# Optimization experiments

Measured on AMD Instinct MI355X. Metric: run time of the kernel, lower is better.

## Reference

```python
import jax, jax.numpy as jnp
import numpy as np

B, D, C = 256, 512, 100000
U_M, L_M = 0.8, 0.45
U_A, L_A = 110.0, 10.0
LAMBDA_G = 35.0
SCALE = 64.0


def setup_inputs() -> dict:
    key = jax.random.key(0)
    k1, k2, k3, k4 = jax.random.split(key, 4)
    x = jax.random.normal(k1, (B, D), dtype=jnp.float32)
    # per-sample feature magnitudes in [l_a, u_a]
    x_norm = L_A + jax.random.uniform(k2, (B, 1), dtype=jnp.float32) * (U_A - L_A)
    labels = jax.random.randint(k3, (B,), 0, C)
    weight = jax.random.normal(k4, (C, D), dtype=jnp.float32)
    return {"x": x, "x_norm": x_norm, "labels": labels, "weight": weight}


def reference(x, x_norm, labels, weight):
    # adaptive margin m(a) = slope * (a - l_a) + l_m, per sample [B,1]
    ada_margin = (U_M - L_M) / (U_A - L_A) * (x_norm - L_A) + L_M
    cos_m = jnp.cos(ada_margin)
    sin_m = jnp.sin(ada_margin)

    xn = x / jnp.linalg.norm(x, axis=-1, keepdims=True)          # [B,D]
    wn = weight / jnp.linalg.norm(weight, axis=-1, keepdims=True)  # [C,D]
    cos_theta = jnp.clip(jnp.einsum('bd,cd->bc', xn, wn), -1.0, 1.0)  # [B,C]
    sin_theta = jnp.sqrt(1.0 - cos_theta * cos_theta)
    cos_theta_m = cos_theta * cos_m - sin_theta * sin_m
    # easy_margin=True: only apply margin where cos_theta > 0
    cos_theta_m = jnp.where(cos_theta > 0, cos_theta_m, cos_theta)

    one_hot = jax.nn.one_hot(labels, C, dtype=cos_theta.dtype)   # [B,C]
    logits = SCALE * (one_hot * cos_theta_m + (1.0 - one_hot) * cos_theta)

    # cross-entropy with mean reduction
    tgt = jnp.take_along_axis(logits, labels[:, None], axis=1)[:, 0]
    ce = jnp.mean(jax.nn.logsumexp(logits, axis=1) - tgt)

    # MagFace G-loss: mean(a / u_a^2 + 1/a)
    loss_g = jnp.mean(x_norm / (U_A * U_A) + 1.0 / x_norm)
    return ce + LAMBDA_G * loss_g
```

## Files before the change

kernel.cpp:

```cpp
#include <hip/hip_runtime.h>
#include <hip/hip_bf16.h>

#define BB 256
#define DD 512
#define CNUM 100000
#define CPAD 100096
#define NCHUNK 782
#define NPART (NCHUNK * 2)

typedef __attribute__((ext_vector_type(8))) short bf16x8;
typedef __attribute__((ext_vector_type(4))) float f32x4;

typedef __attribute__((address_space(1))) void gvoid_t;
typedef __attribute__((address_space(3))) void lvoid_t;

__device__ __forceinline__ void gload16(const void* g, void* l) {
  __builtin_amdgcn_global_load_lds((const gvoid_t*)g, (lvoid_t*)l, 16, 0, 0);
}

__device__ __forceinline__ unsigned short f2bf(float f) {
  union { float f; unsigned int u; } v; v.f = f;
  unsigned int u = v.u;
  unsigned int r = u + 0x7FFFu + ((u >> 16) & 1u);
  return (unsigned short)(r >> 16);
}

__global__ void k_prep_x(const float* __restrict__ x, const float* __restrict__ xnrm,
                         unsigned short* __restrict__ xn, float* __restrict__ cm,
                         float* __restrict__ sm) {
  int b = blockIdx.x;
  int lane = threadIdx.x;
  const float4* xr = (const float4*)(x + (size_t)b * DD);
  float4 v0 = xr[lane * 2];
  float4 v1 = xr[lane * 2 + 1];
  float ss = v0.x * v0.x + v0.y * v0.y + v0.z * v0.z + v0.w * v0.w +
             v1.x * v1.x + v1.y * v1.y + v1.z * v1.z + v1.w * v1.w;
#pragma unroll
  for (int msk = 1; msk < 64; msk <<= 1) ss += __shfl_xor(ss, msk, 64);
  float inv = rsqrtf(ss);
  unsigned int p0 = (unsigned int)f2bf(v0.x * inv) | ((unsigned int)f2bf(v0.y * inv) << 16);
  unsigned int p1 = (unsigned int)f2bf(v0.z * inv) | ((unsigned int)f2bf(v0.w * inv) << 16);
  unsigned int p2 = (unsigned int)f2bf(v1.x * inv) | ((unsigned int)f2bf(v1.y * inv) << 16);
  unsigned int p3 = (unsigned int)f2bf(v1.z * inv) | ((unsigned int)f2bf(v1.w * inv) << 16);
  *(uint4*)(xn + (size_t)b * DD + lane * 8) = make_uint4(p0, p1, p2, p3);
  if (lane == 0) {
    float a = xnrm[b];
    float marg = 0.0035f * (a - 10.0f) + 0.45f;
    cm[b] = cosf(marg);
    sm[b] = sinf(marg);
  }
}

__global__ __launch_bounds__(512) void k_gemm(
    const unsigned short* __restrict__ xn, const float* __restrict__ w,
    const int* __restrict__ labels, const float* __restrict__ cmv,
    const float* __restrict__ smv, float2* __restrict__ part, float* __restrict__ tgt) {
  __shared__ short Xs[BB * 64];
  __shared__ short Ws[128 * 64];
  __shared__ float sInvW[128];
  __shared__ int sLab[BB];
  __shared__ float sCm[BB], sSm[BB];

  int tid = threadIdx.x, wave = tid >> 6, lane = tid & 63;
  int wm = wave >> 1, wq = wave & 1;
  int cbase = blockIdx.x * 128;

  if (tid < BB) {
    sLab[tid] = labels[tid];
    sCm[tid] = cmv[tid];
    sSm[tid] = smv[tid];
  }
  __syncthreads();

  int lr = lane >> 3;
  int lk = (lane & 7) ^ lr;

  int wrow = tid >> 2, wseg = tid & 3;
  int wr_clamped = cbase + wrow;
  if (wr_clamped >= CNUM) wr_clamped = 0;
  const float* wptr = w + (size_t)wr_clamped * DD + wseg * 16;
  float ssacc = 0.0f;
  int wsw0 = wrow * 64 + ((wseg * 16) ^ ((wrow & 7) << 3));
  int wsw1 = wrow * 64 + ((wseg * 16 + 8) ^ ((wrow & 7) << 3));

  f32x4 acc[4][4];
#pragma unroll
  for (int m = 0; m < 4; ++m)
#pragma unroll
    for (int n = 0; n < 4; ++n) acc[m][n] = (f32x4){0.f, 0.f, 0.f, 0.f};

  f32x4 wv[4];
#pragma unroll
  for (int j = 0; j < 4; ++j) wv[j] = *(const f32x4*)(wptr + j * 4);

#pragma unroll
  for (int kc = 0; kc < 8; ++kc) {
    const int k0 = kc * 64;
    asm volatile("s_barrier" ::: "memory");
#pragma unroll
    for (int i = 0; i < 4; ++i) {
      int rbase = i * 64 + wave * 8;
      gload16(xn + (size_t)(rbase + lr) * DD + k0 + lk * 8, &Xs[rbase * 64]);
    }
    asm volatile("s_waitcnt vmcnt(4)" ::: "memory");
    {
      f32x4 a = wv[0], b = wv[1], c = wv[2], d = wv[3];
      ssacc += a[0]*a[0] + a[1]*a[1] + a[2]*a[2] + a[3]*a[3] +
               b[0]*b[0] + b[1]*b[1] + b[2]*b[2] + b[3]*b[3] +
               c[0]*c[0] + c[1]*c[1] + c[2]*c[2] + c[3]*c[3] +
               d[0]*d[0] + d[1]*d[1] + d[2]*d[2] + d[3]*d[3];
      unsigned int q0 = (unsigned int)f2bf(a[0]) | ((unsigned int)f2bf(a[1]) << 16);
      unsigned int q1 = (unsigned int)f2bf(a[2]) | ((unsigned int)f2bf(a[3]) << 16);
      unsigned int q2 = (unsigned int)f2bf(b[0]) | ((unsigned int)f2bf(b[1]) << 16);
      unsigned int q3 = (unsigned int)f2bf(b[2]) | ((unsigned int)f2bf(b[3]) << 16);
      unsigned int q4 = (unsigned int)f2bf(c[0]) | ((unsigned int)f2bf(c[1]) << 16);
      unsigned int q5 = (unsigned int)f2bf(c[2]) | ((unsigned int)f2bf(c[3]) << 16);
      unsigned int q6 = (unsigned int)f2bf(d[0]) | ((unsigned int)f2bf(d[1]) << 16);
      unsigned int q7 = (unsigned int)f2bf(d[2]) | ((unsigned int)f2bf(d[3]) << 16);
      *(uint4*)&Ws[wsw0] = make_uint4(q0, q1, q2, q3);
      *(uint4*)&Ws[wsw1] = make_uint4(q4, q5, q6, q7);
    }
    if (kc < 7) {
#pragma unroll
      for (int j = 0; j < 4; ++j) wv[j] = *(const f32x4*)(wptr + (kc + 1) * 64 + j * 4);
      asm volatile("s_waitcnt vmcnt(4) lgkmcnt(0)" ::: "memory");
    } else {
      asm volatile("s_waitcnt vmcnt(0) lgkmcnt(0)" ::: "memory");
    }
    asm volatile("s_barrier" ::: "memory");
#pragma unroll
    for (int ks = 0; ks < 2; ++ks) {
      int krd = ks * 32 + (lane >> 4) * 8;
      int swz = (lane & 7) << 3;
      bf16x8 af[4], bfr[4];
#pragma unroll
      for (int m = 0; m < 4; ++m) {
        int ra = wm * 64 + m * 16 + (lane & 15);
        af[m] = *(const bf16x8*)&Xs[ra * 64 + (krd ^ swz)];
      }
#pragma unroll
      for (int n = 0; n < 4; ++n) {
        int rb = wq * 64 + n * 16 + (lane & 15);
        bfr[n] = *(const bf16x8*)&Ws[rb * 64 + (krd ^ swz)];
      }
#pragma unroll
      for (int m = 0; m < 4; ++m)
#pragma unroll
        for (int n = 0; n < 4; ++n)
          acc[m][n] = __builtin_amdgcn_mfma_f32_16x16x32_bf16(af[m], bfr[n], acc[m][n], 0, 0, 0);
    }
  }

  ssacc += __shfl_xor(ssacc, 1, 64);
  ssacc += __shfl_xor(ssacc, 2, 64);
  if (wseg == 0) sInvW[wrow] = rsqrtf(ssacc);
  __syncthreads();

  int g = lane >> 4, cb = lane & 15;
  float invc[4];
#pragma unroll
  for (int n = 0; n < 4; ++n) {
    int col = cbase + wq * 64 + n * 16 + cb;
    invc[n] = (col < CNUM) ? sInvW[wq * 64 + n * 16 + cb] : 0.0f;
  }
#pragma unroll
  for (int m = 0; m < 4; ++m) {
#pragma unroll
    for (int r = 0; r < 4; ++r) {
      int row = wm * 64 + m * 16 + g * 4 + r;
      int lab = sLab[row];
      float cmr = sCm[row], smr = sSm[row];
      float lg[4];
      float vmax = -1e30f;
#pragma unroll
      for (int n = 0; n < 4; ++n) {
        int col = cbase + wq * 64 + n * 16 + cb;
        float cv = acc[m][n][r] * invc[n];
        cv = fminf(1.0f, fmaxf(-1.0f, cv));
        float logit;
        if (col == lab) {
          float st = sqrtf(fmaxf(0.0f, 1.0f - cv * cv));
          float cm2 = cv * cmr - st * smr;
          logit = 64.0f * (cv > 0.0f ? cm2 : cv);
          tgt[row] = logit;
        } else {
          logit = 64.0f * cv;
        }
        if (col >= CNUM) logit = -1e30f;
        lg[n] = logit;
        vmax = fmaxf(vmax, logit);
      }
#pragma unroll
      for (int msk = 1; msk < 16; msk <<= 1) vmax = fmaxf(vmax, __shfl_xor(vmax, msk, 64));
      float s = 0.0f;
#pragma unroll
      for (int n = 0; n < 4; ++n) s += __expf(lg[n] - vmax);
#pragma unroll
      for (int msk = 1; msk < 16; msk <<= 1) s += __shfl_xor(s, msk, 64);
      if (cb == 0) part[(size_t)row * NPART + blockIdx.x * 2 + wq] = make_float2(vmax, s);
    }
  }
}

__global__ void k_merge(const float2* __restrict__ part, const float* __restrict__ tgt,
                        float* __restrict__ ce) {
  int b = blockIdx.x, t = threadIdx.x;
  float m = -1e30f, s = 0.0f;
  for (int i = t; i < NPART; i += 256) {
    float2 p = part[(size_t)b * NPART + i];
    float nm = fmaxf(m, p.x);
    s = s * __expf(m - nm) + p.y * __expf(p.x - nm);
    m = nm;
  }
  __shared__ float smx[256], ssm[256];
  smx[t] = m;
  ssm[t] = s;
  __syncthreads();
  for (int off = 128; off > 0; off >>= 1) {
    if (t < off) {
      float m2 = smx[t + off], s2 = ssm[t + off];
      float nm = fmaxf(smx[t], m2);
      ssm[t] = ssm[t] * __expf(smx[t] - nm) + s2 * __expf(m2 - nm);
      smx[t] = nm;
    }
    __syncthreads();
  }
  if (t == 0) ce[b] = smx[0] + logf(ssm[0]) - tgt[b];
}

__global__ void k_final(const float* __restrict__ ce, const float* __restrict__ xnrm,
                        float* __restrict__ out) {
  int t = threadIdx.x;
  float cv = ce[t];
  float a = xnrm[t];
  float gv = a * (1.0f / (110.0f * 110.0f)) + 1.0f / a;
  __shared__ float s1[256], s2[256];
  s1[t] = cv;
  s2[t] = gv;
  __syncthreads();
  for (int off = 128; off > 0; off >>= 1) {
    if (t < off) {
      s1[t] += s1[t + off];
      s2[t] += s2[t + off];
    }
    __syncthreads();
  }
  if (t == 0) out[0] = s1[0] * (1.0f / 256.0f) + 35.0f * s2[0] * (1.0f / 256.0f);
}

extern "C" void kernel_launch(void* const* d_in, const int* in_sizes, int n_in,
                              void* d_out, int out_size, void* d_ws, size_t ws_size,
                              hipStream_t stream) {
  const float* x = (const float*)d_in[0];
  const float* xnrm = (const float*)d_in[1];
  const int* labels = (const int*)d_in[2];
  const float* w = (const float*)d_in[3];

  char* ws = (char*)d_ws;
  unsigned short* XN = (unsigned short*)ws;
  size_t off = (size_t)BB * DD * 2;
  float* CM = (float*)(ws + off);  off += 1024;
  float* SM = (float*)(ws + off);  off += 1024;
  float* TGT = (float*)(ws + off); off += 1024;
  float* CE = (float*)(ws + off);  off += 1024;
  float2* PART = (float2*)(ws + off);

  k_prep_x<<<BB, 64, 0, stream>>>(x, xnrm, XN, CM, SM);
  k_gemm<<<NCHUNK, 512, 0, stream>>>(XN, w, labels, CM, SM, PART, TGT);
  k_merge<<<BB, 256, 0, stream>>>(PART, TGT, CE);
  k_final<<<1, 256, 0, stream>>>(CE, xnrm, (float*)d_out);
}
```

Baseline: 100.5 us.

## Split GEMM over batch halves and double-buffer LDS tiles

The GEMM grid gains a second dimension that splits the 256 batch rows into two 128-row tiles. Each block now computes a 128x128 output tile with 8 waves arranged 2x4, and the number of softmax partials per row doubles. X and W tiles in LDS are double-buffered so the next k-chunk loads while MFMAs run on the current one. The cost is that every W tile is read from global memory and converted to bf16 twice, once per batch half, doubling W traffic, which may dominate because W is large.

Result: no change. 102.1 us (+1.6%).

```diff
diff --git a/kernel.cpp b/kernel.cpp
--- a/kernel.cpp
+++ b/kernel.cpp
@@ -5,8 +5,10 @@
 #define DD 512
 #define CNUM 100000
 #define CPAD 100096
-#define NCHUNK 782
-#define NPART (NCHUNK * 2)
+#define BM 128
+#define BN 128
+#define NCH_N 782
+#define NPART (NCH_N * 4)
 
 typedef __attribute__((ext_vector_type(8))) short bf16x8;
 typedef __attribute__((ext_vector_type(4))) float f32x4;
@@ -55,20 +57,21 @@
     const unsigned short* __restrict__ xn, const float* __restrict__ w,
     const int* __restrict__ labels, const float* __restrict__ cmv,
     const float* __restrict__ smv, float2* __restrict__ part, float* __restrict__ tgt) {
-  __shared__ short Xs[BB * 64];
-  __shared__ short Ws[128 * 64];
-  __shared__ float sInvW[128];
-  __shared__ int sLab[BB];
-  __shared__ float sCm[BB], sSm[BB];
+  __shared__ short Xs[2][BM * 64];
+  __shared__ short Ws[2][BN * 64];
+  __shared__ float sInvW[BN];
+  __shared__ int sLab[BM];
+  __shared__ float sCm[BM], sSm[BM];
 
   int tid = threadIdx.x, wave = tid >> 6, lane = tid & 63;
-  int wm = wave >> 1, wq = wave & 1;
-  int cbase = blockIdx.x * 128;
-
-  if (tid < BB) {
-    sLab[tid] = labels[tid];
-    sCm[tid] = cmv[tid];
-    sSm[tid] = smv[tid];
+  int wm = wave >> 2, wq = wave & 3;
+  int cbase = blockIdx.x * BN;
+  int mbase = blockIdx.y * BM;
+
+  if (tid < BM) {
+    sLab[tid] = labels[mbase + tid];
+    sCm[tid] = cmv[mbase + tid];
+    sSm[tid] = smv[mbase + tid];
   }
   __syncthreads();
 
@@ -76,80 +79,101 @@
   int lk = (lane & 7) ^ lr;
 
   int wrow = tid >> 2, wseg = tid & 3;
-  int wr_clamped = cbase + wrow;
-  if (wr_clamped >= CNUM) wr_clamped = 0;
-  const float* wptr = w + (size_t)wr_clamped * DD + wseg * 16;
+  int wr_c = cbase + wrow;
+  if (wr_c >= CNUM) wr_c = 0;
+  const float* wptr = w + (size_t)wr_c * DD + wseg * 16;
   float ssacc = 0.0f;
   int wsw0 = wrow * 64 + ((wseg * 16) ^ ((wrow & 7) << 3));
   int wsw1 = wrow * 64 + ((wseg * 16 + 8) ^ ((wrow & 7) << 3));
 
-  f32x4 acc[4][4];
+  f32x4 acc[4][2];
 #pragma unroll
   for (int m = 0; m < 4; ++m)
 #pragma unroll
-    for (int n = 0; n < 4; ++n) acc[m][n] = (f32x4){0.f, 0.f, 0.f, 0.f};
+    for (int n = 0; n < 2; ++n) acc[m][n] = (f32x4){0.f, 0.f, 0.f, 0.f};
+
+#define STAGE_X(T, B)                                                          \
+  {                                                                            \
+    const int k0_ = (T) * 64;                                                  \
+    _Pragma("unroll") for (int i = 0; i < 2; ++i) {                            \
+      int rbase = i * 64 + wave * 8;                                           \
+      gload16(xn + (size_t)(mbase + rbase + lr) * DD + k0_ + lk * 8,           \
+              &Xs[B][rbase * 64]);                                             \
+    }                                                                          \
+  }
+
+#define PACK_W(B)                                                              \
+  {                                                                            \
+    f32x4 a = wv[0], b = wv[1], c = wv[2], d = wv[3];                          \
+    ssacc += a[0]*a[0] + a[1]*a[1] + a[2]*a[2] + a[3]*a[3] +                   \
+             b[0]*b[0] + b[1]*b[1] + b[2]*b[2] + b[3]*b[3] +                   \
+             c[0]*c[0] + c[1]*c[1] + c[2]*c[2] + c[3]*c[3] +                   \
+             d[0]*d[0] + d[1]*d[1] + d[2]*d[2] + d[3]*d[3];                    \
+    unsigned int q0 = (unsigned int)f2bf(a[0]) | ((unsigned int)f2bf(a[1]) << 16); \
+    unsigned int q1 = (unsigned int)f2bf(a[2]) | ((unsigned int)f2bf(a[3]) << 16); \
+    unsigned int q2 = (unsigned int)f2bf(b[0]) | ((unsigned int)f2bf(b[1]) << 16); \
+    unsigned int q3 = (unsigned int)f2bf(b[2]) | ((unsigned int)f2bf(b[3]) << 16); \
+    unsigned int q4 = (unsigned int)f2bf(c[0]) | ((unsigned int)f2bf(c[1]) << 16); \
+    unsigned int q5 = (unsigned int)f2bf(c[2]) | ((unsigned int)f2bf(c[3]) << 16); \
+    unsigned int q6 = (unsigned int)f2bf(d[0]) | ((unsigned int)f2bf(d[1]) << 16); \
+    unsigned int q7 = (unsigned int)f2bf(d[2]) | ((unsigned int)f2bf(d[3]) << 16); \
+    *(uint4*)&Ws[B][wsw0] = make_uint4(q0, q1, q2, q3);                        \
+    *(uint4*)&Ws[B][wsw1] = make_uint4(q4, q5, q6, q7);                        \
+  }
+
+#define LOAD_W(T)                                                              \
+  _Pragma("unroll") for (int j = 0; j < 4; ++j)                                \
+      wv[j] = *(const f32x4*)(wptr + (T) * 64 + j * 4);
+
+#define COMPUTE(P)                                                             \
+  _Pragma("unroll") for (int ks = 0; ks < 2; ++ks) {                           \
+    int krd = ks * 32 + (lane >> 4) * 8;                                       \
+    int swz = (lane & 7) << 3;                                                 \
+    bf16x8 af[4], bfr[2];                                                      \
+    _Pragma("unroll") for (int m = 0; m < 4; ++m) {                            \
+      int ra = wm * 64 + m * 16 + (lane & 15);                                 \
+      af[m] = *(const bf16x8*)&Xs[P][ra * 64 + (krd ^ swz)];                   \
+    }                                                                          \
+    _Pragma("unroll") for (int n = 0; n < 2; ++n) {                            \
+      int rb = wq * 32 + n * 16 + (lane & 15);                                 \
+      bfr[n] = *(const bf16x8*)&Ws[P][rb * 64 + (krd ^ swz)];                  \
+    }                                                                          \
+    _Pragma("unroll") for (int m = 0; m < 4; ++m)                              \
+      _Pragma("unroll") for (int n = 0; n < 2; ++n)                            \
+        acc[m][n] = __builtin_amdgcn_mfma_f32_16x16x32_bf16(af[m], bfr[n],     \
+                                                            acc[m][n], 0, 0, 0); \
+  }
 
   f32x4 wv[4];
-#pragma unroll
-  for (int j = 0; j < 4; ++j) wv[j] = *(const f32x4*)(wptr + j * 4);
+  LOAD_W(0);
+  STAGE_X(0, 0);
+  asm volatile("s_waitcnt vmcnt(2)" ::: "memory");
+  PACK_W(0);
+  LOAD_W(1);
+  asm volatile("s_waitcnt vmcnt(4) lgkmcnt(0)" ::: "memory");
+  asm volatile("s_barrier" ::: "memory");
 
 #pragma unroll
   for (int kc = 0; kc < 8; ++kc) {
-    const int k0 = kc * 64;
-    asm volatile("s_barrier" ::: "memory");
-#pragma unroll
-    for (int i = 0; i < 4; ++i) {
-      int rbase = i * 64 + wave * 8;
-      gload16(xn + (size_t)(rbase + lr) * DD + k0 + lk * 8, &Xs[rbase * 64]);
-    }
-    asm volatile("s_waitcnt vmcnt(4)" ::: "memory");
-    {
-      f32x4 a = wv[0], b = wv[1], c = wv[2], d = wv[3];
-      ssacc += a[0]*a[0] + a[1]*a[1] + a[2]*a[2] + a[3]*a[3] +
-               b[0]*b[0] + b[1]*b[1] + b[2]*b[2] + b[3]*b[3] +
-               c[0]*c[0] + c[1]*c[1] + c[2]*c[2] + c[3]*c[3] +
-               d[0]*d[0] + d[1]*d[1] + d[2]*d[2] + d[3]*d[3];
-      unsigned int q0 = (unsigned int)f2bf(a[0]) | ((unsigned int)f2bf(a[1]) << 16);
-      unsigned int q1 = (unsigned int)f2bf(a[2]) | ((unsigned int)f2bf(a[3]) << 16);
-      unsigned int q2 = (unsigned int)f2bf(b[0]) | ((unsigned int)f2bf(b[1]) << 16);
-      unsigned int q3 = (unsigned int)f2bf(b[2]) | ((unsigned int)f2bf(b[3]) << 16);
-      unsigned int q4 = (unsigned int)f2bf(c[0]) | ((unsigned int)f2bf(c[1]) << 16);
-      unsigned int q5 = (unsigned int)f2bf(c[2]) | ((unsigned int)f2bf(c[3]) << 16);
-      unsigned int q6 = (unsigned int)f2bf(d[0]) | ((unsigned int)f2bf(d[1]) << 16);
-      unsigned int q7 = (unsigned int)f2bf(d[2]) | ((unsigned int)f2bf(d[3]) << 16);
-      *(uint4*)&Ws[wsw0] = make_uint4(q0, q1, q2, q3);
-      *(uint4*)&Ws[wsw1] = make_uint4(q4, q5, q6, q7);
-    }
+    const int p = kc & 1;
+    if (kc < 7) STAGE_X(kc + 1, p ^ 1);
+    COMPUTE(p);
     if (kc < 7) {
-#pragma unroll
-      for (int j = 0; j < 4; ++j) wv[j] = *(const f32x4*)(wptr + (kc + 1) * 64 + j * 4);
-      asm volatile("s_waitcnt vmcnt(4) lgkmcnt(0)" ::: "memory");
-    } else {
-      asm volatile("s_waitcnt vmcnt(0) lgkmcnt(0)" ::: "memory");
-    }
-    asm volatile("s_barrier" ::: "memory");
-#pragma unroll
-    for (int ks = 0; ks < 2; ++ks) {
-      int krd = ks * 32 + (lane >> 4) * 8;
-      int swz = (lane & 7) << 3;
-      bf16x8 af[4], bfr[4];
-#pragma unroll
-      for (int m = 0; m < 4; ++m) {
-        int ra = wm * 64 + m * 16 + (lane & 15);
-        af[m] = *(const bf16x8*)&Xs[ra * 64 + (krd ^ swz)];
+      asm volatile("s_waitcnt vmcnt(2)" ::: "memory");
+      PACK_W(p ^ 1);
+      if (kc < 6) {
+        LOAD_W(kc + 2);
+        asm volatile("s_waitcnt vmcnt(4) lgkmcnt(0)" ::: "memory");
+      } else {
+        asm volatile("s_waitcnt vmcnt(0) lgkmcnt(0)" ::: "memory");
       }
-#pragma unroll
-      for (int n = 0; n < 4; ++n) {
-        int rb = wq * 64 + n * 16 + (lane & 15);
-        bfr[n] = *(const bf16x8*)&Ws[rb * 64 + (krd ^ swz)];
-      }
-#pragma unroll
-      for (int m = 0; m < 4; ++m)
-#pragma unroll
-        for (int n = 0; n < 4; ++n)
-          acc[m][n] = __builtin_amdgcn_mfma_f32_16x16x32_bf16(af[m], bfr[n], acc[m][n], 0, 0, 0);
-    }
-  }
+      asm volatile("s_barrier" ::: "memory");
+    }
+  }
+#undef STAGE_X
+#undef PACK_W
+#undef LOAD_W
+#undef COMPUTE
 
   ssacc += __shfl_xor(ssacc, 1, 64);
   ssacc += __shfl_xor(ssacc, 2, 64);
@@ -157,24 +181,25 @@
   __syncthreads();
 
   int g = lane >> 4, cb = lane & 15;
-  float invc[4];
-#pragma unroll
-  for (int n = 0; n < 4; ++n) {
-    int col = cbase + wq * 64 + n * 16 + cb;
-    invc[n] = (col < CNUM) ? sInvW[wq * 64 + n * 16 + cb] : 0.0f;
+  float invc[2];
+#pragma unroll
+  for (int n = 0; n < 2; ++n) {
+    int col = cbase + wq * 32 + n * 16 + cb;
+    invc[n] = (col < CNUM) ? sInvW[wq * 32 + n * 16 + cb] : 0.0f;
   }
 #pragma unroll
   for (int m = 0; m < 4; ++m) {
 #pragma unroll
     for (int r = 0; r < 4; ++r) {
-      int row = wm * 64 + m * 16 + g * 4 + r;
-      int lab = sLab[row];
-      float cmr = sCm[row], smr = sSm[row];
-      float lg[4];
+      int lrow = wm * 64 + m * 16 + g * 4 + r;
+      int grow = mbase + lrow;
+      int lab = sLab[lrow];
+      float cmr = sCm[lrow], smr = sSm[lrow];
+      float lg[2];
       float vmax = -1e30f;
 #pragma unroll
-      for (int n = 0; n < 4; ++n) {
-        int col = cbase + wq * 64 + n * 16 + cb;
+      for (int n = 0; n < 2; ++n) {
+        int col = cbase + wq * 32 + n * 16 + cb;
         float cv = acc[m][n][r] * invc[n];
         cv = fminf(1.0f, fmaxf(-1.0f, cv));
         float logit;
@@ -182,7 +207,7 @@
           float st = sqrtf(fmaxf(0.0f, 1.0f - cv * cv));
           float cm2 = cv * cmr - st * smr;
           logit = 64.0f * (cv > 0.0f ? cm2 : cv);
-          tgt[row] = logit;
+          tgt[grow] = logit;
         } else {
           logit = 64.0f * cv;
         }
@@ -194,10 +219,10 @@
       for (int msk = 1; msk < 16; msk <<= 1) vmax = fmaxf(vmax, __shfl_xor(vmax, msk, 64));
       float s = 0.0f;
 #pragma unroll
-      for (int n = 0; n < 4; ++n) s += __expf(lg[n] - vmax);
+      for (int n = 0; n < 2; ++n) s += __expf(lg[n] - vmax);
 #pragma unroll
       for (int msk = 1; msk < 16; msk <<= 1) s += __shfl_xor(s, msk, 64);
-      if (cb == 0) part[(size_t)row * NPART + blockIdx.x * 2 + wq] = make_float2(vmax, s);
+      if (cb == 0) part[(size_t)grow * NPART + blockIdx.x * 4 + wq] = make_float2(vmax, s);
     }
   }
 }
@@ -266,7 +291,8 @@
   float2* PART = (float2*)(ws + off);
 
   k_prep_x<<<BB, 64, 0, stream>>>(x, xnrm, XN, CM, SM);
-  k_gemm<<<NCHUNK, 512, 0, stream>>>(XN, w, labels, CM, SM, PART, TGT);
+  dim3 grid(NCH_N, BB / BM);
+  k_gemm<<<grid, 512, 0, stream>>>(XN, w, labels, CM, SM, PART, TGT);
   k_merge<<<BB, 256, 0, stream>>>(PART, TGT, CE);
   k_final<<<1, 256, 0, stream>>>(CE, xnrm, (float*)d_out);
 }
```
